# Performance work log

Hardware: AMD Instinct MI355X
Metric: run time of the kernel (lower is better)

The kernel has to match this reference:

```python
import jax, jax.numpy as jnp
import numpy as np

B, S, E, H = 4, 2048, 16, 4  # batch, seq, embed_dim (= n_wires), num_heads
D_K = E // H


def setup_inputs() -> dict:
    key = jax.random.key(0)
    k1, k2, k3, k4, k5 = jax.random.split(key, 5)
    return {
        "x": jax.random.normal(k1, (B, S, E), dtype=jnp.float32),
        "theta": jax.random.normal(k2, (E,), dtype=jnp.float32),
        "Wk": jax.random.normal(k3, (E, E), dtype=jnp.float32) / np.float32(np.sqrt(E)),
        "Wv": jax.random.normal(k4, (E, E), dtype=jnp.float32) / np.float32(np.sqrt(E)),
        "Wc": jax.random.normal(k5, (E, E), dtype=jnp.float32) / np.float32(np.sqrt(E)),
    }


def _split_heads(t):
    # [B, S, E] -> [B, H, S, D_K]
    b, s, _ = t.shape
    return t.reshape(b, s, H, D_K).transpose(0, 2, 1, 3)


def reference(x, theta, Wk, Wv, Wc):
    # Quantum head: RX(x_i) then RX(theta_i) on wire i from |0>, measure PauliZ.
    # Single-qubit RX rotations on disjoint wires factorize: <Z_i> = cos(x_i + theta_i).
    q = jnp.cos(x + theta)          # [B, S, E] (batched over all tokens at once)
    k = x @ Wk.T                    # nn.Linear(bias=False): x @ W^T
    v = x @ Wv.T

    qh, kh, vh = _split_heads(q), _split_heads(k), _split_heads(v)
    scale = np.float32(1.0 / np.sqrt(D_K))
    scores = jnp.einsum("bhqd,bhkd->bhqk", qh, kh) * scale  # [B, H, S, S]
    attn = jax.nn.softmax(scores, axis=-1)
    out = jnp.einsum("bhqk,bhkd->bhqd", attn, vh)           # [B, H, S, D_K]
    out = out.transpose(0, 2, 1, 3).reshape(x.shape)        # [B, S, E]
    return out @ Wc.T
```

## Files before the change

kernel.cpp:

```cpp
#include <hip/hip_runtime.h>
#include <math.h>

#define BB 4
#define SS 2048
#define EE 16
#define HH 4
#define DK 4
#define KS 16
#define NQ (BB*HH*SS)
#define KLEN (SS/KS)
#define QPT 4

#define QSCALE 0.7213475204444817f

__global__ __launch_bounds__(512) void attn_fused(
    const float* __restrict__ x, const float* __restrict__ theta,
    const float* __restrict__ Wk, const float* __restrict__ Wv,
    float* __restrict__ accp, float* __restrict__ lp)
{
    __shared__ float  sx[KLEN * EE];
    __shared__ float4 skv[KLEN * 2];

    int tid = threadIdx.x;
    int ks = blockIdx.x;
    int bh = blockIdx.y;
    int b = bh >> 2;
    int h = bh & 3;

    const float4* xsrc =
        reinterpret_cast<const float4*>(x + ((size_t)b*SS + (size_t)ks*KLEN) * EE);
    reinterpret_cast<float4*>(sx)[tid] = xsrc[tid];

    float th0 = theta[h*4+0], th1 = theta[h*4+1];
    float th2 = theta[h*4+2], th3 = theta[h*4+3];
    float4 qv[QPT];
    #pragma unroll
    for (int j = 0; j < QPT; ++j) {
        int s = tid + j*512;
        float4 xq = *reinterpret_cast<const float4*>(
            x + ((size_t)b*SS + s) * EE + h*4);
        qv[j].x = __cosf(xq.x + th0) * QSCALE;
        qv[j].y = __cosf(xq.y + th1) * QSCALE;
        qv[j].z = __cosf(xq.z + th2) * QSCALE;
        qv[j].w = __cosf(xq.w + th3) * QSCALE;
    }

    __syncthreads();

    if (tid < KLEN) {
        const float4* xr = reinterpret_cast<const float4*>(sx + tid * EE);
        float4 x0 = xr[0], x1 = xr[1], x2 = xr[2], x3 = xr[3];
        float xv[EE] = {x0.x,x0.y,x0.z,x0.w, x1.x,x1.y,x1.z,x1.w,
                        x2.x,x2.y,x2.z,x2.w, x3.x,x3.y,x3.z,x3.w};
        float kd[DK], vd[DK];
        #pragma unroll
        for (int d = 0; d < DK; ++d) {
            float ak = 0.f, av = 0.f;
            #pragma unroll
            for (int e = 0; e < EE; ++e) {
                ak = fmaf(xv[e], Wk[(h*4+d)*EE + e], ak);
                av = fmaf(xv[e], Wv[(h*4+d)*EE + e], av);
            }
            kd[d] = ak; vd[d] = av;
        }
        skv[2*tid]   = make_float4(kd[0], kd[1], kd[2], kd[3]);
        skv[2*tid+1] = make_float4(vd[0], vd[1], vd[2], vd[3]);
    }

    __syncthreads();

    float4 acc[QPT] = {};
    float  lsum[QPT] = {};
    #pragma unroll 8
    for (int s = 0; s < KLEN; ++s) {
        float4 kk = skv[2*s];
        float4 vv = skv[2*s + 1];
        #pragma unroll
        for (int j = 0; j < QPT; ++j) {
            float sc = fmaf(qv[j].x, kk.x, fmaf(qv[j].y, kk.y,
                       fmaf(qv[j].z, kk.z, qv[j].w * kk.w)));
            float p = __builtin_amdgcn_exp2f(sc);
            lsum[j] += p;
            acc[j].x = fmaf(p, vv.x, acc[j].x);
            acc[j].y = fmaf(p, vv.y, acc[j].y);
            acc[j].z = fmaf(p, vv.z, acc[j].z);
            acc[j].w = fmaf(p, vv.w, acc[j].w);
        }
    }

    #pragma unroll
    for (int j = 0; j < QPT; ++j) {
        int gq = bh*SS + tid + j*512;
        *reinterpret_cast<float4*>(accp + ((size_t)ks*NQ + gq)*4) = acc[j];
        lp[(size_t)ks*NQ + gq] = lsum[j];
    }
}

__global__ __launch_bounds__(64) void out_kernel(
    const float* __restrict__ accp, const float* __restrict__ lp,
    const float* __restrict__ Wc, float* __restrict__ out)
{
    int t = blockIdx.x * 64 + threadIdx.x;
    int b = t >> 11;
    int s = t & (SS - 1);

    float attn[EE];
    #pragma unroll
    for (int h = 0; h < HH; ++h) {
        int gq = (b*HH + h)*SS + s;
        float ax = 0.f, ay = 0.f, az = 0.f, aw = 0.f, l = 0.f;
        #pragma unroll
        for (int ks = 0; ks < KS; ++ks) {
            float4 a = *reinterpret_cast<const float4*>(accp + ((size_t)ks*NQ + gq)*4);
            ax += a.x; ay += a.y; az += a.z; aw += a.w;
            l += lp[(size_t)ks*NQ + gq];
        }
        float inv = 1.0f / l;
        attn[h*4+0] = ax*inv; attn[h*4+1] = ay*inv;
        attn[h*4+2] = az*inv; attn[h*4+3] = aw*inv;
    }

    float4* orow = reinterpret_cast<float4*>(out + (size_t)t * EE);
    #pragma unroll
    for (int e4 = 0; e4 < 4; ++e4) {
        float o[4];
        #pragma unroll
        for (int i = 0; i < 4; ++i) {
            int e = e4*4 + i;
            float acc = 0.f;
            #pragma unroll
            for (int j = 0; j < EE; ++j)
                acc = fmaf(attn[j], Wc[e*EE + j], acc);
            o[i] = acc;
        }
        orow[e4] = make_float4(o[0], o[1], o[2], o[3]);
    }
}

extern "C" void kernel_launch(void* const* d_in, const int* in_sizes, int n_in,
                              void* d_out, int out_size, void* d_ws, size_t ws_size,
                              hipStream_t stream)
{
    const float* x     = (const float*)d_in[0];
    const float* theta = (const float*)d_in[1];
    const float* Wk    = (const float*)d_in[2];
    const float* Wv    = (const float*)d_in[3];
    const float* Wc    = (const float*)d_in[4];
    float* out = (float*)d_out;

    float* ws   = (float*)d_ws;
    float* accp = ws;
    float* lp   = accp + (size_t)KS*NQ*4;

    attn_fused<<<dim3(KS, BB*HH), 512, 0, stream>>>(x, theta, Wk, Wv, accp, lp);
    out_kernel<<<dim3((BB*SS)/64), 64, 0, stream>>>(accp, lp, Wc, out);
}
```

Measured before the change: 92.48 us.

## Use packed FP32 math with SoA K/V and rebalanced query/key split

Restructures the attention kernel so each block handles half the queries for a longer key slice: the key splits drop from 16 to 8 and queries per thread from 4 to 2, with a new grid dimension over query chunks. K/V are stored in LDS as struct-of-arrays and read as float4, so the inner loop processes pairs of keys with two-wide vector FMAs that can map to packed FP32 instructions. The x staging through shared memory is removed, and halving the number of partial results also reduces the reads in the combine kernel. The cost is more register pressure, and the number of exp2 evaluations per thread is unchanged.

```diff
diff --git a/kernel.cpp b/kernel.cpp
--- a/kernel.cpp
+++ b/kernel.cpp
@@ -6,49 +6,33 @@
 #define EE 16
 #define HH 4
 #define DK 4
-#define KS 16
+#define KS 8
 #define NQ (BB*HH*SS)
 #define KLEN (SS/KS)
-#define QPT 4
+#define QPT 2
 
 #define QSCALE 0.7213475204444817f
+
+typedef float v2f __attribute__((ext_vector_type(2)));
 
 __global__ __launch_bounds__(512) void attn_fused(
     const float* __restrict__ x, const float* __restrict__ theta,
     const float* __restrict__ Wk, const float* __restrict__ Wv,
     float* __restrict__ accp, float* __restrict__ lp)
 {
-    __shared__ float  sx[KLEN * EE];
-    __shared__ float4 skv[KLEN * 2];
+    __shared__ float skx[KLEN], sky[KLEN], skz[KLEN], skw[KLEN];
+    __shared__ float svx[KLEN], svy[KLEN], svz[KLEN], svw[KLEN];
 
     int tid = threadIdx.x;
-    int ks = blockIdx.x;
-    int bh = blockIdx.y;
+    int qc = blockIdx.x;
+    int ks = blockIdx.y;
+    int bh = blockIdx.z;
     int b = bh >> 2;
     int h = bh & 3;
 
-    const float4* xsrc =
-        reinterpret_cast<const float4*>(x + ((size_t)b*SS + (size_t)ks*KLEN) * EE);
-    reinterpret_cast<float4*>(sx)[tid] = xsrc[tid];
-
-    float th0 = theta[h*4+0], th1 = theta[h*4+1];
-    float th2 = theta[h*4+2], th3 = theta[h*4+3];
-    float4 qv[QPT];
-    #pragma unroll
-    for (int j = 0; j < QPT; ++j) {
-        int s = tid + j*512;
-        float4 xq = *reinterpret_cast<const float4*>(
-            x + ((size_t)b*SS + s) * EE + h*4);
-        qv[j].x = __cosf(xq.x + th0) * QSCALE;
-        qv[j].y = __cosf(xq.y + th1) * QSCALE;
-        qv[j].z = __cosf(xq.z + th2) * QSCALE;
-        qv[j].w = __cosf(xq.w + th3) * QSCALE;
-    }
-
-    __syncthreads();
-
     if (tid < KLEN) {
-        const float4* xr = reinterpret_cast<const float4*>(sx + tid * EE);
+        const float4* xr = reinterpret_cast<const float4*>(
+            x + ((size_t)b*SS + (size_t)ks*KLEN + tid) * EE);
         float4 x0 = xr[0], x1 = xr[1], x2 = xr[2], x3 = xr[3];
         float xv[EE] = {x0.x,x0.y,x0.z,x0.w, x1.x,x1.y,x1.z,x1.w,
                         x2.x,x2.y,x2.z,x2.w, x3.x,x3.y,x3.z,x3.w};
@@ -63,37 +47,94 @@
             }
             kd[d] = ak; vd[d] = av;
         }
-        skv[2*tid]   = make_float4(kd[0], kd[1], kd[2], kd[3]);
-        skv[2*tid+1] = make_float4(vd[0], vd[1], vd[2], vd[3]);
+        skx[tid] = kd[0]; sky[tid] = kd[1]; skz[tid] = kd[2]; skw[tid] = kd[3];
+        svx[tid] = vd[0]; svy[tid] = vd[1]; svz[tid] = vd[2]; svw[tid] = vd[3];
     }
+
+    float th0 = theta[h*4+0], th1 = theta[h*4+1];
+    float th2 = theta[h*4+2], th3 = theta[h*4+3];
+    int s0 = qc*1024 + tid;
+    float4 xq0 = *reinterpret_cast<const float4*>(x + ((size_t)b*SS + s0) * EE + h*4);
+    float4 xq1 = *reinterpret_cast<const float4*>(x + ((size_t)b*SS + s0 + 512) * EE + h*4);
+    float q0x = __cosf(xq0.x + th0) * QSCALE, q0y = __cosf(xq0.y + th1) * QSCALE;
+    float q0z = __cosf(xq0.z + th2) * QSCALE, q0w = __cosf(xq0.w + th3) * QSCALE;
+    float q1x = __cosf(xq1.x + th0) * QSCALE, q1y = __cosf(xq1.y + th1) * QSCALE;
+    float q1z = __cosf(xq1.z + th2) * QSCALE, q1w = __cosf(xq1.w + th3) * QSCALE;
+    v2f Q0x = {q0x,q0x}, Q0y = {q0y,q0y}, Q0z = {q0z,q0z}, Q0w = {q0w,q0w};
+    v2f Q1x = {q1x,q1x}, Q1y = {q1y,q1y}, Q1z = {q1z,q1z}, Q1w = {q1w,q1w};
 
     __syncthreads();
 
-    float4 acc[QPT] = {};
-    float  lsum[QPT] = {};
-    #pragma unroll 8
-    for (int s = 0; s < KLEN; ++s) {
-        float4 kk = skv[2*s];
-        float4 vv = skv[2*s + 1];
-        #pragma unroll
-        for (int j = 0; j < QPT; ++j) {
-            float sc = fmaf(qv[j].x, kk.x, fmaf(qv[j].y, kk.y,
-                       fmaf(qv[j].z, kk.z, qv[j].w * kk.w)));
-            float p = __builtin_amdgcn_exp2f(sc);
-            lsum[j] += p;
-            acc[j].x = fmaf(p, vv.x, acc[j].x);
-            acc[j].y = fmaf(p, vv.y, acc[j].y);
-            acc[j].z = fmaf(p, vv.z, acc[j].z);
-            acc[j].w = fmaf(p, vv.w, acc[j].w);
-        }
+    v2f a0x = {}, a0y = {}, a0z = {}, a0w = {};
+    v2f a1x = {}, a1y = {}, a1z = {}, a1w = {};
+    v2f l0 = {}, l1 = {};
+    const float4* kx4 = reinterpret_cast<const float4*>(skx);
+    const float4* ky4 = reinterpret_cast<const float4*>(sky);
+    const float4* kz4 = reinterpret_cast<const float4*>(skz);
+    const float4* kw4 = reinterpret_cast<const float4*>(skw);
+    const float4* vx4 = reinterpret_cast<const float4*>(svx);
+    const float4* vy4 = reinterpret_cast<const float4*>(svy);
+    const float4* vz4 = reinterpret_cast<const float4*>(svz);
+    const float4* vw4 = reinterpret_cast<const float4*>(svw);
+
+    #pragma unroll 2
+    for (int i = 0; i < KLEN/4; ++i) {
+        float4 kx = kx4[i], ky = ky4[i], kz = kz4[i], kw = kw4[i];
+        float4 vx = vx4[i], vy = vy4[i], vz = vz4[i], vw = vw4[i];
+        v2f kx01 = {kx.x, kx.y}, kx23 = {kx.z, kx.w};
+        v2f ky01 = {ky.x, ky.y}, ky23 = {ky.z, ky.w};
+        v2f kz01 = {kz.x, kz.y}, kz23 = {kz.z, kz.w};
+        v2f kw01 = {kw.x, kw.y}, kw23 = {kw.z, kw.w};
+        v2f vx01 = {vx.x, vx.y}, vx23 = {vx.z, vx.w};
+        v2f vy01 = {vy.x, vy.y}, vy23 = {vy.z, vy.w};
+        v2f vz01 = {vz.x, vz.y}, vz23 = {vz.z, vz.w};
+        v2f vw01 = {vw.x, vw.y}, vw23 = {vw.z, vw.w};
+
+        v2f sc = __builtin_elementwise_fma(Q0x, kx01,
+                 __builtin_elementwise_fma(Q0y, ky01,
+                 __builtin_elementwise_fma(Q0z, kz01, Q0w * kw01)));
+        v2f p; p.x = __builtin_amdgcn_exp2f(sc.x); p.y = __builtin_amdgcn_exp2f(sc.y);
+        l0 += p;
+        a0x = __builtin_elementwise_fma(p, vx01, a0x);
+        a0y = __builtin_elementwise_fma(p, vy01, a0y);
+        a0z = __builtin_elementwise_fma(p, vz01, a0z);
+        a0w = __builtin_elementwise_fma(p, vw01, a0w);
+        sc = __builtin_elementwise_fma(Q0x, kx23,
+             __builtin_elementwise_fma(Q0y, ky23,
+             __builtin_elementwise_fma(Q0z, kz23, Q0w * kw23)));
+        p.x = __builtin_amdgcn_exp2f(sc.x); p.y = __builtin_amdgcn_exp2f(sc.y);
+        l0 += p;
+        a0x = __builtin_elementwise_fma(p, vx23, a0x);
+        a0y = __builtin_elementwise_fma(p, vy23, a0y);
+        a0z = __builtin_elementwise_fma(p, vz23, a0z);
+        a0w = __builtin_elementwise_fma(p, vw23, a0w);
+        sc = __builtin_elementwise_fma(Q1x, kx01,
+             __builtin_elementwise_fma(Q1y, ky01,
+             __builtin_elementwise_fma(Q1z, kz01, Q1w * kw01)));
+        p.x = __builtin_amdgcn_exp2f(sc.x); p.y = __builtin_amdgcn_exp2f(sc.y);
+        l1 += p;
+        a1x = __builtin_elementwise_fma(p, vx01, a1x);
+        a1y = __builtin_elementwise_fma(p, vy01, a1y);
+        a1z = __builtin_elementwise_fma(p, vz01, a1z);
+        a1w = __builtin_elementwise_fma(p, vw01, a1w);
+        sc = __builtin_elementwise_fma(Q1x, kx23,
+             __builtin_elementwise_fma(Q1y, ky23,
+             __builtin_elementwise_fma(Q1z, kz23, Q1w * kw23)));
+        p.x = __builtin_amdgcn_exp2f(sc.x); p.y = __builtin_amdgcn_exp2f(sc.y);
+        l1 += p;
+        a1x = __builtin_elementwise_fma(p, vx23, a1x);
+        a1y = __builtin_elementwise_fma(p, vy23, a1y);
+        a1z = __builtin_elementwise_fma(p, vz23, a1z);
+        a1w = __builtin_elementwise_fma(p, vw23, a1w);
     }
 
-    #pragma unroll
-    for (int j = 0; j < QPT; ++j) {
-        int gq = bh*SS + tid + j*512;
-        *reinterpret_cast<float4*>(accp + ((size_t)ks*NQ + gq)*4) = acc[j];
-        lp[(size_t)ks*NQ + gq] = lsum[j];
-    }
+    int gq0 = bh*SS + s0;
+    *reinterpret_cast<float4*>(accp + ((size_t)ks*NQ + gq0)*4) =
+        make_float4(a0x.x + a0x.y, a0y.x + a0y.y, a0z.x + a0z.y, a0w.x + a0w.y);
+    lp[(size_t)ks*NQ + gq0] = l0.x + l0.y;
+    *reinterpret_cast<float4*>(accp + ((size_t)ks*NQ + gq0 + 512)*4) =
+        make_float4(a1x.x + a1x.y, a1y.x + a1y.y, a1z.x + a1z.y, a1w.x + a1w.y);
+    lp[(size_t)ks*NQ + gq0 + 512] = l1.x + l1.y;
 }
 
 __global__ __launch_bounds__(64) void out_kernel(
@@ -152,6 +193,6 @@
     float* accp = ws;
     float* lp   = accp + (size_t)KS*NQ*4;
 
-    attn_fused<<<dim3(KS, BB*HH), 512, 0, stream>>>(x, theta, Wk, Wv, accp, lp);
+    attn_fused<<<dim3(2, KS, BB*HH), 512, 0, stream>>>(x, theta, Wk, Wv, accp, lp);
     out_kernel<<<dim3((BB*SS)/64), 64, 0, stream>>>(accp, lp, Wc, out);
 }
```

After: 84.51 us. 8.6% less time.
